# Kernel tuning notes

Hardware: AMD Instinct MI355X
Metric: run time of the kernel (lower is better)

Reference implementation:

```python
import jax, jax.numpy as jnp
import numpy as np
from jax import lax

T, B, D, H, C, G = 32, 512, 1024, 2048, 10, 16
BETA = 0.95
THRESH = 1.0


def _build_mask(key, out_f, in_f, p_intra=1.0, p_inter=0.15):
    ig, og = in_f // G, out_f // G
    same = (jnp.arange(out_f) // og)[:, None] == (jnp.arange(in_f) // ig)[None, :]
    probs = jnp.where(same, p_intra, p_inter)
    return (jax.random.uniform(key, (out_f, in_f)) < probs).astype(jnp.float32)


def setup_inputs() -> dict:
    key = jax.random.key(0)
    ks = jax.random.split(key, 12)
    def w(k, out_f, in_f):
        return jax.random.normal(k, (out_f, in_f), jnp.float32) * (1.0 / np.sqrt(in_f))
    return {
        'x_seq': jax.random.normal(ks[0], (T, B, D), jnp.float32),
        'w1': w(ks[1], H, D), 'b1': jax.random.normal(ks[2], (H,), jnp.float32) * 0.01,
        'mask1': _build_mask(ks[3], H, D),
        'w2': w(ks[4], H, H), 'b2': jax.random.normal(ks[5], (H,), jnp.float32) * 0.01,
        'mask2': _build_mask(ks[6], H, H),
        'w3': w(ks[7], H, H), 'b3': jax.random.normal(ks[8], (H,), jnp.float32) * 0.01,
        'mask3': _build_mask(ks[9], H, H),
        'w_out': w(ks[10], C, H), 'b_out': jax.random.normal(ks[11], (C,), jnp.float32) * 0.01,
    }


@jax.custom_vjp
def spike(x):
    # heaviside fire, fast_sigmoid(slope=25) surrogate gradient
    return (x > 0).astype(x.dtype)

def _spike_fwd(x):
    return spike(x), x

def _spike_bwd(x, g):
    return (g / (25.0 * jnp.abs(x) + 1.0) ** 2,)

spike.defvjp(_spike_fwd, _spike_bwd)


def _lif(cur, mem):
    # snntorch Leaky (reset-by-subtraction): reset from previous mem (detached)
    reset = lax.stop_gradient((mem > THRESH).astype(cur.dtype))
    mem = BETA * mem + cur - reset * THRESH
    spk = spike(mem - THRESH)
    return spk, mem


def reference(x_seq, w1, b1, mask1, w2, b2, mask2, w3, b3, mask3, w_out, b_out):
    # cache masked weights once (same math as per-step weight*mask)
    ew1, ew2, ew3 = w1 * mask1, w2 * mask2, w3 * mask3
    Bsz = x_seq.shape[1]
    mem1 = jnp.zeros((Bsz, H), x_seq.dtype)
    mem2 = jnp.zeros((Bsz, H), x_seq.dtype)
    mem3 = jnp.zeros((Bsz, H), x_seq.dtype)
    mem_o = jnp.zeros((Bsz, C), x_seq.dtype)
    ssum = jnp.zeros((Bsz, C), x_seq.dtype)

    def step(carry, x_t):
        mem1, mem2, mem3, mem_o, ssum = carry
        spk1, mem1 = _lif(x_t @ ew1.T + b1, mem1)
        spk2, mem2 = _lif(spk1 @ ew2.T + b2, mem2)
        spk3, mem3 = _lif(spk2 @ ew3.T + b3, mem3)
        spk_o, mem_o = _lif(spk3 @ w_out.T + b_out, mem_o)
        return (mem1, mem2, mem3, mem_o, ssum + spk_o), None

    (mem1, mem2, mem3, mem_o, ssum), _ = lax.scan(step, (mem1, mem2, mem3, mem_o, ssum), x_seq)
    return ssum
```

## Files before the change

kernel.cpp:

```cpp
#include <hip/hip_runtime.h>

#define TSTEPS 32
#define BSZ    512
#define DIN    1024
#define HID    2048
#define NCLS   10
#define BETA   0.95f
#define VTH    1.0f
#define SPKB   ((size_t)BSZ * (HID / 8))

typedef __attribute__((ext_vector_type(4))) float          f4;
typedef __attribute__((ext_vector_type(4))) float          f32x4;
typedef __attribute__((ext_vector_type(8))) __bf16         bf16x8;
typedef __attribute__((ext_vector_type(8))) unsigned short us8;
typedef __attribute__((ext_vector_type(4))) unsigned short us4;
typedef __attribute__((ext_vector_type(2))) unsigned int   u32x2;

__device__ inline unsigned short f2bf(float f) {
    unsigned u = __float_as_uint(f);
    u += 0x7FFF + ((u >> 16) & 1);
    return (unsigned short)(u >> 16);
}
__device__ inline float bf2f(unsigned short h) {
    return __uint_as_float(((unsigned)h) << 16);
}

__device__ __forceinline__ void split_f4pair(f4 v0, f4 v1, us8& o0, us8& o1, us8& o2) {
#pragma unroll
    for (int jj = 0; jj < 4; jj++) {
        float v = v0[jj];
        unsigned short h1 = f2bf(v); float r = v - bf2f(h1);
        unsigned short h2 = f2bf(r); float r2 = r - bf2f(h2);
        o0[jj] = h1; o1[jj] = h2; o2[jj] = f2bf(r2);
        v = v1[jj];
        h1 = f2bf(v); r = v - bf2f(h1);
        h2 = f2bf(r); r2 = r - bf2f(h2);
        o0[jj + 4] = h1; o1[jj + 4] = h2; o2[jj + 4] = f2bf(r2);
    }
}

__global__ __launch_bounds__(256)
void split3(const float* __restrict__ w, const float* __restrict__ m,
            unsigned short* __restrict__ h1, unsigned short* __restrict__ h2,
            unsigned short* __restrict__ h3, int n4)
{
    int i      = blockIdx.x * blockDim.x + threadIdx.x;
    int stride = gridDim.x * blockDim.x;
    for (; i < n4; i += stride) {
        f4 wv = ((const f4*)w)[i];
        f4 mv = ((const f4*)m)[i];
        us4 a, b, c;
#pragma unroll
        for (int j = 0; j < 4; j++) {
            float e  = wv[j] * mv[j];
            unsigned short x1 = f2bf(e);
            float r  = e - bf2f(x1);
            unsigned short x2 = f2bf(r);
            float r2 = r - bf2f(x2);
            a[j] = x1; b[j] = x2; c[j] = f2bf(r2);
        }
        ((us4*)h1)[i] = a;
        ((us4*)h2)[i] = b;
        ((us4*)h3)[i] = c;
    }
}

__global__ __launch_bounds__(256)
void split3q(const float* __restrict__ w, const float* __restrict__ m,
             unsigned short* __restrict__ q)
{
    const int NK = HID * HID;
    int gid = blockIdx.x * 256 + threadIdx.x;
    const int lane = gid & 63;
    const int t    = gid >> 6;
    const int kt   = t & (HID / 32 - 1);
    const int nt   = t >> 6;
    const int n = nt * 16 + (lane & 15);
    const int k = kt * 32 + (lane >> 4) * 8;
    const size_t src = (size_t)n * HID + k;
    f4 w0 = *(const f4*)(w + src),     w1v = *(const f4*)(w + src + 4);
    f4 m0 = *(const f4*)(m + src),     m1v = *(const f4*)(m + src + 4);
    us8 q0, q1, q2;
    split_f4pair(w0 * m0, w1v * m1v, q0, q1, q2);
    ((us8*)q)[gid]            = q0;
    ((us8*)(q + NK))[gid]     = q1;
    ((us8*)(q + 2 * NK))[gid] = q2;
}

__global__ __launch_bounds__(256)
void zerof(float* __restrict__ p, int n4)
{
    int i      = blockIdx.x * blockDim.x + threadIdx.x;
    int stride = gridDim.x * blockDim.x;
    f4 z = {0.f, 0.f, 0.f, 0.f};
    for (; i < n4; i += stride) ((f4*)p)[i] = z;
}

__device__ __forceinline__ void xsplit_dev(const float* __restrict__ xt,
                                           unsigned short* __restrict__ dst,
                                           int bid, int nblk, int tid)
{
    const int n4 = BSZ * DIN / 4;
    const int PS = BSZ * DIN;
    int i      = bid * 256 + tid;
    int stride = nblk * 256;
    for (; i < n4; i += stride) {
        f4 v = ((const f4*)xt)[i];
        us4 a, b, c;
#pragma unroll
        for (int j = 0; j < 4; j++) {
            float e = v[j];
            unsigned short x1 = f2bf(e);
            float r  = e - bf2f(x1);
            unsigned short x2 = f2bf(r);
            float r2 = r - bf2f(x2);
            a[j] = x1; b[j] = x2; c[j] = f2bf(r2);
        }
        ((us4*)(dst))[i]          = a;
        ((us4*)(dst + PS))[i]     = b;
        ((us4*)(dst + 2 * PS))[i] = c;
    }
}

__global__ __launch_bounds__(256)
void xsplit_k(const float* __restrict__ xt, unsigned short* __restrict__ dst)
{
    xsplit_dev(xt, dst, blockIdx.x, gridDim.x, threadIdx.x);
}

__device__ __forceinline__ void lif_epi(const f32x4 acc[2][2], const float* __restrict__ bias,
                                        float* __restrict__ memOut, unsigned char* __restrict__ sbits,
                                        int bm, int bn, int wm, int wn, int lane)
{
    const int fr = lane & 15;
#pragma unroll
    for (int fm = 0; fm < 2; fm++)
#pragma unroll
        for (int fn = 0; fn < 2; fn++) {
            const int n  = bn * 64 + wn * 32 + fn * 16 + fr;
            const float bv = bias[n];
            const int rbase = bm * 64 + wm * 32 + fm * 16 + (lane >> 4) * 4;
#pragma unroll
            for (int r = 0; r < 4; r++) {
                const int row = rbase + r;
                float* mp = memOut + (size_t)row * HID + n;
                float mo  = *mp;
                float m2  = BETA * mo + (acc[fm][fn][r] + bv) - ((mo > VTH) ? VTH : 0.f);
                *mp = m2;
                unsigned long long bal = __ballot(m2 > VTH);
                if (fr == 0) {
                    unsigned short bits = (unsigned short)(bal >> ((lane >> 4) * 16));
                    *(unsigned short*)(sbits + (size_t)row * (HID / 8) + bn * 8 + wn * 4 + fn * 2) = bits;
                }
            }
        }
}

__device__ __forceinline__ void lif_epi4b(const f32x4 (&acc)[4], const float* __restrict__ bias,
                                          float* __restrict__ memOut,
                                          unsigned char* __restrict__ sbitsOut,
                                          int bm, int bn, int wv, int lane)
{
    const int fr = lane & 15;
    const int n  = bn * 64 + wv * 16 + fr;
    const float bv = bias[n];
#pragma unroll
    for (int fm = 0; fm < 4; fm++) {
        const int rbase = bm * 64 + fm * 16 + (lane >> 4) * 4;
#pragma unroll
        for (int r = 0; r < 4; r++) {
            const int row = rbase + r;
            float* mp = memOut + (size_t)row * HID + n;
            float mo  = *mp;
            float m2  = BETA * mo + (acc[fm][r] + bv) - ((mo > VTH) ? VTH : 0.f);
            *mp = m2;
            unsigned long long bal = __ballot(m2 > VTH);
            if (fr == 0) {
                unsigned short bits = (unsigned short)(bal >> ((lane >> 4) * 16));
                *(unsigned short*)(sbitsOut + (size_t)row * (HID / 8) + bn * 8 + wv * 2) = bits;
            }
        }
    }
}

__device__ __forceinline__ void role_out_b(const unsigned char* __restrict__ sbits,
    const float* __restrict__ wo, const float* __restrict__ bo,
    float* __restrict__ memo, float* __restrict__ ssum, int b, int lane)
{
    const unsigned int bits = *(const unsigned int*)(sbits + (size_t)b * (HID / 8) + lane * 4);
    float acc[NCLS];
#pragma unroll
    for (int c = 0; c < NCLS; c++) {
        const f4* wrow = (const f4*)(wo + (size_t)c * HID + lane * 32);
        float s = 0.f;
#pragma unroll
        for (int q = 0; q < 8; q++) {
            f4 w = wrow[q];
#pragma unroll
            for (int i = 0; i < 4; i++)
                if ((bits >> (q * 4 + i)) & 1u) s += w[i];
        }
        acc[c] = s;
    }
#pragma unroll
    for (int c = 0; c < NCLS; c++)
#pragma unroll
        for (int m = 1; m < 64; m <<= 1) acc[c] += __shfl_xor(acc[c], m, 64);

    if (lane == 0) {
#pragma unroll
        for (int c = 0; c < NCLS; c++) {
            float mo  = memo[b * NCLS + c];
            float rst = (mo > VTH) ? VTH : 0.f;
            float m2  = BETA * mo + acc[c] + bo[c] - rst;
            memo[b * NCLS + c] = m2;
            if (m2 > VTH) ssum[b * NCLS + c] += 1.f;
        }
    }
}

__device__ __forceinline__ void role_l23b(unsigned char* smem,
    const unsigned char* __restrict__ sbitsIn,
    const unsigned short* __restrict__ Bp,
    const float* __restrict__ bias, float* __restrict__ memOut,
    unsigned char* __restrict__ sbitsOut, int rb, int tid)
{
    auto Bs = reinterpret_cast<unsigned short(*)[3][64 * 40]>(smem);
    const size_t PS = (size_t)HID * HID;

    const int bn = rb & 31, bm = rb >> 5;
    const int srow = tid >> 2, skq = tid & 3;
    const int lane = tid & 63, wv = tid >> 6;
    const int wm = wv >> 1, wn = wv & 1;
    const int fr = lane & 15, fk = (lane >> 4) * 8;
    const size_t bRow = (size_t)(bn * 64 + srow) * HID;
    const int sdst = srow * 40 + skq * 8;

    const unsigned char* aP0 = sbitsIn + (size_t)(bm * 64 + wm * 32 + fr) * (HID / 8);
    const unsigned char* aP1 = aP0 + (size_t)16 * (HID / 8);

    f32x4 acc[2][2] = {};
    us8 bb0, bb1, bb2;
    unsigned aw0, aw1;

    auto ldB = [&](int k0) {
        bb0 = *(const us8*)(Bp + bRow + k0 + skq * 8);
        bb1 = *(const us8*)(Bp + PS + bRow + k0 + skq * 8);
        bb2 = *(const us8*)(Bp + 2 * PS + bRow + k0 + skq * 8);
    };
    auto stage = [&](int nb) {
        *(us8*)&Bs[nb][0][sdst] = bb0;
        *(us8*)&Bs[nb][1][sdst] = bb1;
        *(us8*)&Bs[nb][2][sdst] = bb2;
    };

    ldB(0); stage(0);
    aw0 = *(const unsigned*)(aP0);
    aw1 = *(const unsigned*)(aP1);
    __syncthreads();

    const int nsteps = HID / 32;
    for (int s = 0; s < nsteps; s++) {
        const int buf = s & 1;
        const bool more = (s + 1 < nsteps);
        unsigned awn0 = 0, awn1 = 0;
        if (more) {
            ldB((s + 1) * 32);
            awn0 = *(const unsigned*)(aP0 + (s + 1) * 4);
            awn1 = *(const unsigned*)(aP1 + (s + 1) * 4);
        }

        bf16x8 af[2];
        {
            unsigned byt0 = aw0 >> fk, byt1 = aw1 >> fk;
            us8 e0, e1;
#pragma unroll
            for (int jj = 0; jj < 8; jj++) {
                e0[jj] = ((byt0 >> jj) & 1u) ? (unsigned short)0x3F80 : (unsigned short)0;
                e1[jj] = ((byt1 >> jj) & 1u) ? (unsigned short)0x3F80 : (unsigned short)0;
            }
            af[0] = *(bf16x8*)&e0;
            af[1] = *(bf16x8*)&e1;
        }

        bf16x8 bf[3][2];
#pragma unroll
        for (int fn = 0; fn < 2; fn++) {
            bf[0][fn] = *(const bf16x8*)&Bs[buf][0][(wn * 32 + fn * 16 + fr) * 40 + fk];
            bf[1][fn] = *(const bf16x8*)&Bs[buf][1][(wn * 32 + fn * 16 + fr) * 40 + fk];
            bf[2][fn] = *(const bf16x8*)&Bs[buf][2][(wn * 32 + fn * 16 + fr) * 40 + fk];
        }
#pragma unroll
        for (int fm = 0; fm < 2; fm++)
#pragma unroll
            for (int fn = 0; fn < 2; fn++) {
                acc[fm][fn] = __builtin_amdgcn_mfma_f32_16x16x32_bf16(af[fm], bf[0][fn], acc[fm][fn], 0, 0, 0);
                acc[fm][fn] = __builtin_amdgcn_mfma_f32_16x16x32_bf16(af[fm], bf[1][fn], acc[fm][fn], 0, 0, 0);
                acc[fm][fn] = __builtin_amdgcn_mfma_f32_16x16x32_bf16(af[fm], bf[2][fn], acc[fm][fn], 0, 0, 0);
            }

        if (more) { stage(buf ^ 1); aw0 = awn0; aw1 = awn1; }
        __syncthreads();
    }

    lif_epi(acc, bias, memOut, sbitsOut, bm, bn, wm, wn, lane);
}

__device__ __forceinline__ void role_l1p(unsigned char* smem,
    const unsigned short* __restrict__ Ap,
    const unsigned short* __restrict__ Wp,
    const float* __restrict__ bias, float* __restrict__ memOut,
    unsigned char* __restrict__ sbitsOut, int rb, int tid)
{
    auto As = reinterpret_cast<unsigned short(*)[64 * 40]>(smem);
    auto Bs = reinterpret_cast<unsigned short(*)[3][64 * 40]>(smem + 15360);
    const size_t APS = (size_t)BSZ * DIN;
    const size_t BPS = (size_t)HID * DIN;

    const int bn = rb & 31, bm = rb >> 5;
    const int srow = tid >> 2, skq = tid & 3;
    const int lane = tid & 63, wv = tid >> 6;
    const int wm = wv >> 1, wn = wv & 1;
    const int fr = lane & 15, fk = (lane >> 4) * 8;
    const size_t aRow = (size_t)(bm * 64 + srow) * DIN;
    const size_t bRow = (size_t)(bn * 64 + srow) * DIN;
    const int sdst = srow * 40 + skq * 8;

    f32x4 acc[2][2] = {};
    us8 aa0, aa1, aa2, bb0, bb1, bb2;

    auto ldnext = [&](int k0) {
        aa0 = *(const us8*)(Ap + aRow + k0 + skq * 8);
        aa1 = *(const us8*)(Ap + APS + aRow + k0 + skq * 8);
        aa2 = *(const us8*)(Ap + 2 * APS + aRow + k0 + skq * 8);
        bb0 = *(const us8*)(Wp + bRow + k0 + skq * 8);
        bb1 = *(const us8*)(Wp + BPS + bRow + k0 + skq * 8);
        bb2 = *(const us8*)(Wp + 2 * BPS + bRow + k0 + skq * 8);
    };
    auto stageA = [&]() {
        *(us8*)&As[0][sdst] = aa0;
        *(us8*)&As[1][sdst] = aa1;
        *(us8*)&As[2][sdst] = aa2;
    };
    auto stageB = [&](int nb) {
        *(us8*)&Bs[nb][0][sdst] = bb0;
        *(us8*)&Bs[nb][1][sdst] = bb1;
        *(us8*)&Bs[nb][2][sdst] = bb2;
    };

    ldnext(0); stageA(); stageB(0);
    __syncthreads();

    const int nsteps = DIN / 32;
    for (int s = 0; s < nsteps; s++) {
        const bool more = (s + 1 < nsteps);
        if (more) ldnext((s + 1) * 32);

        bf16x8 af[3][2], bf[3][2];
#pragma unroll
        for (int p = 0; p < 3; p++)
#pragma unroll
            for (int f = 0; f < 2; f++) {
                af[p][f] = *(const bf16x8*)&As[p][(wm * 32 + f * 16 + fr) * 40 + fk];
                bf[p][f] = *(const bf16x8*)&Bs[s & 1][p][(wn * 32 + f * 16 + fr) * 40 + fk];
            }
#pragma unroll
        for (int pa = 0; pa < 3; pa++)
#pragma unroll
            for (int pb = 0; pb < 3; pb++) {
                if (pa + pb <= 2) {
#pragma unroll
                    for (int fm = 0; fm < 2; fm++)
#pragma unroll
                        for (int fn = 0; fn < 2; fn++)
                            acc[fm][fn] = __builtin_amdgcn_mfma_f32_16x16x32_bf16(
                                af[pa][fm], bf[pb][fn], acc[fm][fn], 0, 0, 0);
                }
            }

        __syncthreads();
        if (more) { stageA(); stageB((s + 1) & 1); }
        __syncthreads();
    }

    lif_epi(acc, bias, memOut, sbitsOut, bm, bn, wm, wn, lane);
}

__global__ __launch_bounds__(256)
void snn_step2(const float* __restrict__ x,
               unsigned short* __restrict__ xp,
               const unsigned short* __restrict__ w1p, const float* __restrict__ b1,
               const unsigned short* __restrict__ w2p, const float* __restrict__ b2,
               const unsigned short* __restrict__ w3p, const float* __restrict__ b3,
               const float* __restrict__ wo, const float* __restrict__ bo,
               float* __restrict__ mem1, float* __restrict__ mem2, float* __restrict__ mem3,
               float* __restrict__ memo,
               unsigned char* __restrict__ spk1, unsigned char* __restrict__ spk2,
               unsigned char* __restrict__ spk3,
               float* __restrict__ ssum, int j)
{
    __shared__ __align__(16) unsigned char smem[46080];
    const int bid = blockIdx.x, tid = threadIdx.x;
    const size_t XSLOT = (size_t)3 * BSZ * DIN;

    if (bid < 256) {
        const int t = j;
        if (t <= TSTEPS - 1)
            role_l1p(smem, xp + (size_t)(t & 1) * XSLOT, w1p, b1, mem1,
                     spk1 + (size_t)(t & 1) * SPKB, bid, tid);
    } else if (bid < 512) {
        const int t = j - 1;
        if (t >= 0 && t <= TSTEPS - 1)
            role_l23b(smem, spk1 + (size_t)(t & 1) * SPKB, w2p, b2, mem2,
                      spk2 + (size_t)(t & 1) * SPKB, bid - 256, tid);
    } else if (bid < 768) {
        const int t = j - 2;
        if (t >= 0 && t <= TSTEPS - 1)
            role_l23b(smem, spk2 + (size_t)(t & 1) * SPKB, w3p, b3, mem3,
                      spk3 + (size_t)(t & 1) * SPKB, bid - 512, tid);
    } else {
        const int t1 = j + 1;
        if (t1 <= TSTEPS - 1)
            xsplit_dev(x + (size_t)t1 * BSZ * DIN,
                       xp + (size_t)(t1 & 1) * XSLOT, bid - 768, 128, tid);
        const int t = j - 3;
        if (t >= 0 && t <= TSTEPS - 1) {
            const int lane = tid & 63, wvi = tid >> 6;
            role_out_b(spk3 + (size_t)(t & 1) * SPKB, wo, bo, memo, ssum,
                       (bid - 768) * 4 + wvi, lane);
        }
    }
}


__device__ __forceinline__ void role_l23e(unsigned char* smem,
    const unsigned char* __restrict__ sbitsIn,
    const unsigned short* __restrict__ Bq,
    const float* __restrict__ bias, float* __restrict__ memOut,
    unsigned char* __restrict__ sbitsOut, int rb, int tid)
{
    u32x2* lut = (u32x2*)smem;
    if (tid < 16) {
        u32x2 e;
        e.x = ((tid & 1) ? 0x3F80u : 0u) | ((tid & 2) ? 0x3F800000u : 0u);
        e.y = ((tid & 4) ? 0x3F80u : 0u) | ((tid & 8) ? 0x3F800000u : 0u);
        lut[tid] = e;
    }
    __syncthreads();

    const int bn = rb & 31, bm = rb >> 5;
    const int lane = tid & 63, wv = tid >> 6;
    const int fr = lane & 15, fk = (lane >> 4) * 8;

    const size_t PSQ = (size_t)HID * HID / 8;
    const us8* bP0 = (const us8*)Bq + (size_t)(bn * 4 + wv) * (HID / 32) * 64 + lane;
    const us8* bP1 = bP0 + PSQ;
    const us8* bP2 = bP1 + PSQ;

    const unsigned char* aR = sbitsIn + (size_t)(bm * 64 + fr) * (HID / 8);

    f32x4 acc[4] = {};
    us8 bb[2][3];
    us4 awq[2][4];

#define LDB4(SET, S) do { const int sc_ = (S) < 64 ? (S) : 63;                 \
        bb[SET][0] = bP0[sc_ * 64];                                            \
        bb[SET][1] = bP1[sc_ * 64];                                            \
        bb[SET][2] = bP2[sc_ * 64]; } while (0)

#define LDA4(SET, G) do { const int gc_ = (G) < 16 ? (G) : 15;                 \
        awq[SET][0] = *(const us4*)(aR + 0 * 16 * (HID / 8) + gc_ * 16);       \
        awq[SET][1] = *(const us4*)(aR + 1 * 16 * (HID / 8) + gc_ * 16);       \
        awq[SET][2] = *(const us4*)(aR + 2 * 16 * (HID / 8) + gc_ * 16);       \
        awq[SET][3] = *(const us4*)(aR + 3 * 16 * (HID / 8) + gc_ * 16); } while (0)

#define EXPAND(AF, W) do { unsigned by_ = ((W) >> fk) & 0xFFu;                 \
        u32x2 lo_ = lut[by_ & 15u];                                            \
        u32x2 hi_ = lut[by_ >> 4];                                             \
        ((u32x2*)&(AF))[0] = lo_;                                              \
        ((u32x2*)&(AF))[1] = hi_; } while (0)

#define STEP(BSET, ASET, COMP) do {                                            \
        us8 a0_, a1_, a2_, a3_;                                                \
        EXPAND(a0_, awq[ASET][0][COMP]);                                       \
        EXPAND(a1_, awq[ASET][1][COMP]);                                       \
        EXPAND(a2_, awq[ASET][2][COMP]);                                       \
        EXPAND(a3_, awq[ASET][3][COMP]);                                       \
        bf16x8 b0_ = *(const bf16x8*)&bb[BSET][0];                             \
        bf16x8 b1_ = *(const bf16x8*)&bb[BSET][1];                             \
        bf16x8 b2_ = *(const bf16x8*)&bb[BSET][2];                             \
        bf16x8 fa0_ = *(const bf16x8*)&a0_;                                    \
        bf16x8 fa1_ = *(const bf16x8*)&a1_;                                    \
        bf16x8 fa2_ = *(const bf16x8*)&a2_;                                    \
        bf16x8 fa3_ = *(const bf16x8*)&a3_;                                    \
        acc[0] = __builtin_amdgcn_mfma_f32_16x16x32_bf16(fa0_, b0_, acc[0], 0, 0, 0); \
        acc[0] = __builtin_amdgcn_mfma_f32_16x16x32_bf16(fa0_, b1_, acc[0], 0, 0, 0); \
        acc[0] = __builtin_amdgcn_mfma_f32_16x16x32_bf16(fa0_, b2_, acc[0], 0, 0, 0); \
        acc[1] = __builtin_amdgcn_mfma_f32_16x16x32_bf16(fa1_, b0_, acc[1], 0, 0, 0); \
        acc[1] = __builtin_amdgcn_mfma_f32_16x16x32_bf16(fa1_, b1_, acc[1], 0, 0, 0); \
        acc[1] = __builtin_amdgcn_mfma_f32_16x16x32_bf16(fa1_, b2_, acc[1], 0, 0, 0); \
        acc[2] = __builtin_amdgcn_mfma_f32_16x16x32_bf16(fa2_, b0_, acc[2], 0, 0, 0); \
        acc[2] = __builtin_amdgcn_mfma_f32_16x16x32_bf16(fa2_, b1_, acc[2], 0, 0, 0); \
        acc[2] = __builtin_amdgcn_mfma_f32_16x16x32_bf16(fa2_, b2_, acc[2], 0, 0, 0); \
        acc[3] = __builtin_amdgcn_mfma_f32_16x16x32_bf16(fa3_, b0_, acc[3], 0, 0, 0); \
        acc[3] = __builtin_amdgcn_mfma_f32_16x16x32_bf16(fa3_, b1_, acc[3], 0, 0, 0); \
        acc[3] = __builtin_amdgcn_mfma_f32_16x16x32_bf16(fa3_, b2_, acc[3], 0, 0, 0); \
    } while (0)

    LDB4(0, 0); LDB4(1, 1);
    LDA4(0, 0); LDA4(1, 1);

    for (int g = 0; g < 16; g += 2) {
        const int s0 = g * 4;
        STEP(0, 0, 0); LDB4(0, s0 + 2);
        STEP(1, 0, 1); LDB4(1, s0 + 3);
        STEP(0, 0, 2); LDB4(0, s0 + 4);
        STEP(1, 0, 3); LDB4(1, s0 + 5);
        LDA4(0, g + 2);
        STEP(0, 1, 0); LDB4(0, s0 + 6);
        STEP(1, 1, 1); LDB4(1, s0 + 7);
        STEP(0, 1, 2); LDB4(0, s0 + 8);
        STEP(1, 1, 3); LDB4(1, s0 + 9);
        LDA4(1, g + 3);
    }

#undef LDB4
#undef LDA4
#undef EXPAND
#undef STEP

    lif_epi4b(acc, bias, memOut, sbitsOut, bm, bn, wv, lane);
}

__device__ __forceinline__ void role_l1s(unsigned char* smem,
    const unsigned short* __restrict__ Ap,
    const unsigned short* __restrict__ Wp,
    const float* __restrict__ bias, float* __restrict__ memOut,
    unsigned char* __restrict__ sbitsOut, int rb, int tid)
{
    auto As = reinterpret_cast<unsigned short(*)[64 * 40]>(smem);
    auto Bs = reinterpret_cast<unsigned short(*)[64 * 40]>(smem + 15360);
    const size_t APS = (size_t)BSZ * DIN;
    const size_t BPS = (size_t)HID * DIN;

    const int bn = rb & 31, bm = rb >> 5;
    const int srow = tid >> 2, skq = tid & 3;
    const int lane = tid & 63, wv = tid >> 6;
    const int wm = wv >> 1, wn = wv & 1;
    const int fr = lane & 15, fk = (lane >> 4) * 8;
    const size_t aRow = (size_t)(bm * 64 + srow) * DIN;
    const size_t bRow = (size_t)(bn * 64 + srow) * DIN;
    const int sdst = srow * 40 + skq * 8;

    f32x4 acc[2][2] = {};
    us8 aa0, aa1, aa2, bb0, bb1, bb2;

    auto ldnext = [&](int k0) {
        aa0 = *(const us8*)(Ap + aRow + k0 + skq * 8);
        aa1 = *(const us8*)(Ap + APS + aRow + k0 + skq * 8);
        aa2 = *(const us8*)(Ap + 2 * APS + aRow + k0 + skq * 8);
        bb0 = *(const us8*)(Wp + bRow + k0 + skq * 8);
        bb1 = *(const us8*)(Wp + BPS + bRow + k0 + skq * 8);
        bb2 = *(const us8*)(Wp + 2 * BPS + bRow + k0 + skq * 8);
    };
    auto stageAB = [&]() {
        *(us8*)&As[0][sdst] = aa0;
        *(us8*)&As[1][sdst] = aa1;
        *(us8*)&As[2][sdst] = aa2;
        *(us8*)&Bs[0][sdst] = bb0;
        *(us8*)&Bs[1][sdst] = bb1;
        *(us8*)&Bs[2][sdst] = bb2;
    };

    ldnext(0); stageAB();
    __syncthreads();

    const int nsteps = DIN / 32;
    for (int s = 0; s < nsteps; s++) {
        const bool more = (s + 1 < nsteps);
        if (more) ldnext((s + 1) * 32);

        bf16x8 af[3][2], bf[3][2];
#pragma unroll
        for (int p = 0; p < 3; p++)
#pragma unroll
            for (int f = 0; f < 2; f++) {
                af[p][f] = *(const bf16x8*)&As[p][(wm * 32 + f * 16 + fr) * 40 + fk];
                bf[p][f] = *(const bf16x8*)&Bs[p][(wn * 32 + f * 16 + fr) * 40 + fk];
            }
#pragma unroll
        for (int pa = 0; pa < 3; pa++)
#pragma unroll
            for (int pb = 0; pb < 3; pb++) {
                if (pa + pb <= 2) {
#pragma unroll
                    for (int fm = 0; fm < 2; fm++)
#pragma unroll
                        for (int fn = 0; fn < 2; fn++)
                            acc[fm][fn] = __builtin_amdgcn_mfma_f32_16x16x32_bf16(
                                af[pa][fm], bf[pb][fn], acc[fm][fn], 0, 0, 0);
                }
            }

        __syncthreads();
        if (more) stageAB();
        __syncthreads();
    }

    lif_epi(acc, bias, memOut, sbitsOut, bm, bn, wm, wn, lane);
}

__global__ __launch_bounds__(256, 4)
void snn_step4(const float* __restrict__ x,
               unsigned short* __restrict__ xp,
               const unsigned short* __restrict__ w1p, const float* __restrict__ b1,
               const unsigned short* __restrict__ w2q, const float* __restrict__ b2,
               const unsigned short* __restrict__ w3q, const float* __restrict__ b3,
               const float* __restrict__ wo, const float* __restrict__ bo,
               float* __restrict__ mem1, float* __restrict__ mem2, float* __restrict__ mem3,
               float* __restrict__ memo,
               unsigned char* __restrict__ spk1, unsigned char* __restrict__ spk2,
               unsigned char* __restrict__ spk3,
               float* __restrict__ ssum, int j)
{
    __shared__ __align__(16) unsigned char smem[30720];
    const int bid = blockIdx.x, tid = threadIdx.x;
    const size_t XSLOT = (size_t)3 * BSZ * DIN;

    if (bid < 256) {
        const int t = j;
        if (t <= TSTEPS - 1)
            role_l1s(smem, xp + (size_t)(t & 1) * XSLOT, w1p, b1, mem1,
                     spk1 + (size_t)(t & 1) * SPKB, bid, tid);
    } else if (bid < 512) {
        const int t = j - 1;
        if (t >= 0 && t <= TSTEPS - 1)
            role_l23e(smem, spk1 + (size_t)(t & 1) * SPKB, w2q, b2, mem2,
                      spk2 + (size_t)(t & 1) * SPKB, bid - 256, tid);
    } else if (bid < 768) {
        const int t = j - 2;
        if (t >= 0 && t <= TSTEPS - 1)
            role_l23e(smem, spk2 + (size_t)(t & 1) * SPKB, w3q, b3, mem3,
                      spk3 + (size_t)(t & 1) * SPKB, bid - 512, tid);
    } else {
        const int t1 = j + 1;
        if (t1 <= TSTEPS - 1)
            xsplit_dev(x + (size_t)t1 * BSZ * DIN,
                       xp + (size_t)(t1 & 1) * XSLOT, bid - 768, 256, tid);
        const int t = j - 3;
        if (t >= 0 && t <= TSTEPS - 1) {
            const int lane = tid & 63, wvi = tid >> 6;
            if (wvi < 2)
                role_out_b(spk3 + (size_t)(t & 1) * SPKB, wo, bo, memo, ssum,
                           (bid - 768) * 2 + wvi, lane);
        }
    }
}

extern "C" void kernel_launch(void* const* d_in, const int* in_sizes, int n_in,
                              void* d_out, int out_size, void* d_ws, size_t ws_size,
                              hipStream_t stream)
{
    const float* x  = (const float*)d_in[0];
    const float* w1 = (const float*)d_in[1];
    const float* b1 = (const float*)d_in[2];
    const float* m1 = (const float*)d_in[3];
    const float* w2 = (const float*)d_in[4];
    const float* b2 = (const float*)d_in[5];
    const float* m2 = (const float*)d_in[6];
    const float* w3 = (const float*)d_in[7];
    const float* b3 = (const float*)d_in[8];
    const float* m3 = (const float*)d_in[9];
    const float* wo = (const float*)d_in[10];
    const float* bo = (const float*)d_in[11];
    float* out = (float*)d_out;

    const size_t planeB  = (size_t)HID * HID * 2;
    const size_t plane1B = (size_t)HID * DIN * 2;
    const size_t planeXB = (size_t)BSZ * DIN * 2;
    const size_t memB    = (size_t)BSZ * HID * 4;
    const size_t memoB   = (size_t)BSZ * NCLS * 4;
    const size_t spk2B   = 2 * SPKB;

    unsigned char* base = (unsigned char*)d_ws;

    const size_t needV4 = 6 * planeB + 3 * plane1B + 6 * planeXB
                        + 3 * memB + memoB + 3 * spk2B + 4096;

    const int nW1  = HID * DIN / 4;
    const size_t HH = (size_t)HID * HID;
    const size_t HD = (size_t)HID * DIN;

    if (ws_size >= needV4) {
        unsigned short* w2q = (unsigned short*)base;
        unsigned short* w3q = (unsigned short*)(base + 3 * planeB);
        unsigned short* w1p = (unsigned short*)(base + 6 * planeB);
        unsigned short* xp  = (unsigned short*)(base + 6 * planeB + 3 * plane1B);
        unsigned char* mbase = base + 6 * planeB + 3 * plane1B + 6 * planeXB;
        float* mem1 = (float*)(mbase);
        float* mem2 = (float*)(mbase + memB);
        float* mem3 = (float*)(mbase + 2 * memB);
        float* memo = (float*)(mbase + 3 * memB);
        unsigned char* spk1 = mbase + 3 * memB + memoB;
        unsigned char* spk2 = spk1 + spk2B;
        unsigned char* spk3 = spk2 + spk2B;

        split3q<<<2048, 256, 0, stream>>>(w2, m2, w2q);
        split3q<<<2048, 256, 0, stream>>>(w3, m3, w3q);
        split3<<<1024, 256, 0, stream>>>(w1, m1, w1p, w1p + HD, w1p + 2 * HD, nW1);
        xsplit_k<<<256, 256, 0, stream>>>(x, xp);

        zerof<<<1024, 256, 0, stream>>>(mem1, (int)((3 * memB + memoB) / 16));
        zerof<<<8, 256, 0, stream>>>(out, (BSZ * NCLS) / 4);

        for (int j = 0; j <= TSTEPS + 2; j++) {
            snn_step4<<<1024, 256, 0, stream>>>(x, xp, w1p, b1, w2q, b2, w3q, b3,
                                                wo, bo, mem1, mem2, mem3, memo,
                                                spk1, spk2, spk3, out, j);
        }
        return;
    }

    const size_t needV2 = 6 * planeB + 3 * plane1B + 6 * planeXB
                        + 3 * memB + memoB + 3 * spk2B;
    if (ws_size < needV2) return;

    unsigned short* w2p = (unsigned short*)base;
    unsigned short* w3p = (unsigned short*)(base + 3 * planeB);
    unsigned short* w1p = (unsigned short*)(base + 6 * planeB);
    unsigned short* xp  = (unsigned short*)(base + 6 * planeB + 3 * plane1B);
    unsigned char* mbase = base + 6 * planeB + 3 * plane1B + 6 * planeXB;
    float* mem1 = (float*)(mbase);
    float* mem2 = (float*)(mbase + memB);
    float* mem3 = (float*)(mbase + 2 * memB);
    float* memo = (float*)(mbase + 3 * memB);
    unsigned char* spk1 = mbase + 3 * memB + memoB;
    unsigned char* spk2 = spk1 + spk2B;
    unsigned char* spk3 = spk2 + spk2B;

    const int nW23 = HID * HID / 4;
    split3<<<1024, 256, 0, stream>>>(w2, m2, w2p, w2p + HH, w2p + 2 * HH, nW23);
    split3<<<1024, 256, 0, stream>>>(w3, m3, w3p, w3p + HH, w3p + 2 * HH, nW23);
    split3<<<1024, 256, 0, stream>>>(w1, m1, w1p, w1p + HD, w1p + 2 * HD, nW1);
    xsplit_k<<<256, 256, 0, stream>>>(x, xp);

    zerof<<<1024, 256, 0, stream>>>(mem1, (int)((3 * memB + memoB) / 16));
    zerof<<<8, 256, 0, stream>>>(out, (BSZ * NCLS) / 4);

    for (int j = 0; j <= TSTEPS + 2; j++) {
        snn_step2<<<896, 256, 0, stream>>>(x, xp, w1p, b1, w2p, b2, w3p, b3,
                                           wo, bo, mem1, mem2, mem3, memo,
                                           spk1, spk2, spk3, out, j);
    }
}
```

Measured before the change: 1.738 ms.

## Halve layer-2/3 tile height, prefragment x for direct MFMA loads, raise occupancy

Layers 2 and 3 now use 32-row tiles, so their block count doubles to 512 per layer and the grid grows to 1536 blocks, with launch bounds raised to 6 blocks per CU. The spike-bit inner loop is restructured to load 32-bit words per 32-wide K step and expand them through the LUT. The x split now writes a layout matching the MFMA fragments, so layer 1 reads A directly from global memory instead of staging it in LDS, which halves shared memory. This targets more parallelism and less LDS traffic, at the cost of lower reuse of the B operand per block and more global A reads.

Result: slower. 3.177 ms (+82.8%).

```diff
diff --git a/kernel.cpp b/kernel.cpp
--- a/kernel.cpp
+++ b/kernel.cpp
@@ -128,6 +128,35 @@
     xsplit_dev(xt, dst, blockIdx.x, gridDim.x, threadIdx.x);
 }
 
+__device__ __forceinline__ void xsplitq_dev(const float* __restrict__ xt,
+                                            unsigned short* __restrict__ dstu,
+                                            int bid, int tid)
+{
+    us8* dst = (us8*)dstu;
+    const int gid  = bid * 256 + tid;
+    const int lane = gid & 63;
+    const int t2   = gid >> 6;
+    const int kt   = t2 & 31;
+    const int rt   = t2 >> 5;
+    const int n = rt * 16 + (lane & 15);
+    const int k = kt * 32 + (lane >> 4) * 8;
+    const size_t src = (size_t)n * DIN + k;
+    f4 v0 = *(const f4*)(xt + src);
+    f4 v1 = *(const f4*)(xt + src + 4);
+    us8 q0, q1, q2;
+    split_f4pair(v0, v1, q0, q1, q2);
+    const size_t XPS = (size_t)BSZ * DIN / 8;
+    dst[gid]            = q0;
+    dst[XPS + gid]      = q1;
+    dst[2 * XPS + gid]  = q2;
+}
+
+__global__ __launch_bounds__(256)
+void xsplitq_k(const float* __restrict__ xt, unsigned short* __restrict__ dst)
+{
+    xsplitq_dev(xt, dst, blockIdx.x, threadIdx.x);
+}
+
 __device__ __forceinline__ void lif_epi(const f32x4 acc[2][2], const float* __restrict__ bias,
                                         float* __restrict__ memOut, unsigned char* __restrict__ sbits,
                                         int bm, int bn, int wm, int wn, int lane)
@@ -156,7 +185,7 @@
         }
 }
 
-__device__ __forceinline__ void lif_epi4b(const f32x4 (&acc)[4], const float* __restrict__ bias,
+__device__ __forceinline__ void lif_epi2b(const f32x4 (&acc)[2], const float* __restrict__ bias,
                                           float* __restrict__ memOut,
                                           unsigned char* __restrict__ sbitsOut,
                                           int bm, int bn, int wv, int lane)
@@ -165,8 +194,8 @@
     const int n  = bn * 64 + wv * 16 + fr;
     const float bv = bias[n];
 #pragma unroll
-    for (int fm = 0; fm < 4; fm++) {
-        const int rbase = bm * 64 + fm * 16 + (lane >> 4) * 4;
+    for (int fm = 0; fm < 2; fm++) {
+        const int rbase = bm * 32 + fm * 16 + (lane >> 4) * 4;
 #pragma unroll
         for (int r = 0; r < 4; r++) {
             const int row = rbase + r;
@@ -433,7 +462,7 @@
 }
 
 
-__device__ __forceinline__ void role_l23e(unsigned char* smem,
+__device__ __forceinline__ void role_l23g(unsigned char* smem,
     const unsigned char* __restrict__ sbitsIn,
     const unsigned short* __restrict__ Bq,
     const float* __restrict__ bias, float* __restrict__ memOut,
@@ -457,137 +486,123 @@
     const us8* bP1 = bP0 + PSQ;
     const us8* bP2 = bP1 + PSQ;
 
-    const unsigned char* aR = sbitsIn + (size_t)(bm * 64 + fr) * (HID / 8);
-
-    f32x4 acc[4] = {};
-    us8 bb[2][3];
-    us4 awq[2][4];
-
-#define LDB4(SET, S) do { const int sc_ = (S) < 64 ? (S) : 63;                 \
-        bb[SET][0] = bP0[sc_ * 64];                                            \
-        bb[SET][1] = bP1[sc_ * 64];                                            \
-        bb[SET][2] = bP2[sc_ * 64]; } while (0)
-
-#define LDA4(SET, G) do { const int gc_ = (G) < 16 ? (G) : 15;                 \
-        awq[SET][0] = *(const us4*)(aR + 0 * 16 * (HID / 8) + gc_ * 16);       \
-        awq[SET][1] = *(const us4*)(aR + 1 * 16 * (HID / 8) + gc_ * 16);       \
-        awq[SET][2] = *(const us4*)(aR + 2 * 16 * (HID / 8) + gc_ * 16);       \
-        awq[SET][3] = *(const us4*)(aR + 3 * 16 * (HID / 8) + gc_ * 16); } while (0)
-
-#define EXPAND(AF, W) do { unsigned by_ = ((W) >> fk) & 0xFFu;                 \
+    const unsigned char* aP0 = sbitsIn + (size_t)(bm * 32 + fr) * (HID / 8);
+    const unsigned char* aP1 = aP0 + (size_t)16 * (HID / 8);
+
+    f32x4 acc[2] = {};
+    us8 bbA0, bbA1, bbA2, bbB0, bbB1, bbB2;
+    unsigned awA0, awA1, awB0, awB1;
+    us8 afA0, afA1, afB0, afB1;
+
+#define LDBA_(S) do { const int sc_ = (S) < 64 ? (S) : 63;                     \
+        bbA0 = bP0[sc_ * 64]; bbA1 = bP1[sc_ * 64]; bbA2 = bP2[sc_ * 64]; } while (0)
+#define LDBB_(S) do { const int sc_ = (S) < 64 ? (S) : 63;                     \
+        bbB0 = bP0[sc_ * 64]; bbB1 = bP1[sc_ * 64]; bbB2 = bP2[sc_ * 64]; } while (0)
+#define LDAWA_(S) do { const int sc_ = (S) < 64 ? (S) : 63;                    \
+        awA0 = *(const unsigned*)(aP0 + sc_ * 4);                              \
+        awA1 = *(const unsigned*)(aP1 + sc_ * 4); } while (0)
+#define LDAWB_(S) do { const int sc_ = (S) < 64 ? (S) : 63;                    \
+        awB0 = *(const unsigned*)(aP0 + sc_ * 4);                              \
+        awB1 = *(const unsigned*)(aP1 + sc_ * 4); } while (0)
+#define EXPW_(AF, W) do { unsigned by_ = ((W) >> fk) & 0xFFu;                  \
         u32x2 lo_ = lut[by_ & 15u];                                            \
         u32x2 hi_ = lut[by_ >> 4];                                             \
         ((u32x2*)&(AF))[0] = lo_;                                              \
         ((u32x2*)&(AF))[1] = hi_; } while (0)
-
-#define STEP(BSET, ASET, COMP) do {                                            \
-        us8 a0_, a1_, a2_, a3_;                                                \
-        EXPAND(a0_, awq[ASET][0][COMP]);                                       \
-        EXPAND(a1_, awq[ASET][1][COMP]);                                       \
-        EXPAND(a2_, awq[ASET][2][COMP]);                                       \
-        EXPAND(a3_, awq[ASET][3][COMP]);                                       \
-        bf16x8 b0_ = *(const bf16x8*)&bb[BSET][0];                             \
-        bf16x8 b1_ = *(const bf16x8*)&bb[BSET][1];                             \
-        bf16x8 b2_ = *(const bf16x8*)&bb[BSET][2];                             \
-        bf16x8 fa0_ = *(const bf16x8*)&a0_;                                    \
-        bf16x8 fa1_ = *(const bf16x8*)&a1_;                                    \
-        bf16x8 fa2_ = *(const bf16x8*)&a2_;                                    \
-        bf16x8 fa3_ = *(const bf16x8*)&a3_;                                    \
-        acc[0] = __builtin_amdgcn_mfma_f32_16x16x32_bf16(fa0_, b0_, acc[0], 0, 0, 0); \
-        acc[0] = __builtin_amdgcn_mfma_f32_16x16x32_bf16(fa0_, b1_, acc[0], 0, 0, 0); \
-        acc[0] = __builtin_amdgcn_mfma_f32_16x16x32_bf16(fa0_, b2_, acc[0], 0, 0, 0); \
-        acc[1] = __builtin_amdgcn_mfma_f32_16x16x32_bf16(fa1_, b0_, acc[1], 0, 0, 0); \
-        acc[1] = __builtin_amdgcn_mfma_f32_16x16x32_bf16(fa1_, b1_, acc[1], 0, 0, 0); \
-        acc[1] = __builtin_amdgcn_mfma_f32_16x16x32_bf16(fa1_, b2_, acc[1], 0, 0, 0); \
-        acc[2] = __builtin_amdgcn_mfma_f32_16x16x32_bf16(fa2_, b0_, acc[2], 0, 0, 0); \
-        acc[2] = __builtin_amdgcn_mfma_f32_16x16x32_bf16(fa2_, b1_, acc[2], 0, 0, 0); \
-        acc[2] = __builtin_amdgcn_mfma_f32_16x16x32_bf16(fa2_, b2_, acc[2], 0, 0, 0); \
-        acc[3] = __builtin_amdgcn_mfma_f32_16x16x32_bf16(fa3_, b0_, acc[3], 0, 0, 0); \
-        acc[3] = __builtin_amdgcn_mfma_f32_16x16x32_bf16(fa3_, b1_, acc[3], 0, 0, 0); \
-        acc[3] = __builtin_amdgcn_mfma_f32_16x16x32_bf16(fa3_, b2_, acc[3], 0, 0, 0); \
-    } while (0)
-
-    LDB4(0, 0); LDB4(1, 1);
-    LDA4(0, 0); LDA4(1, 1);
-
-    for (int g = 0; g < 16; g += 2) {
-        const int s0 = g * 4;
-        STEP(0, 0, 0); LDB4(0, s0 + 2);
-        STEP(1, 0, 1); LDB4(1, s0 + 3);
-        STEP(0, 0, 2); LDB4(0, s0 + 4);
-        STEP(1, 0, 3); LDB4(1, s0 + 5);
-        LDA4(0, g + 2);
-        STEP(0, 1, 0); LDB4(0, s0 + 6);
-        STEP(1, 1, 1); LDB4(1, s0 + 7);
-        STEP(0, 1, 2); LDB4(0, s0 + 8);
-        STEP(1, 1, 3); LDB4(1, s0 + 9);
-        LDA4(1, g + 3);
-    }
-
-#undef LDB4
-#undef LDA4
-#undef EXPAND
-#undef STEP
-
-    lif_epi4b(acc, bias, memOut, sbitsOut, bm, bn, wv, lane);
-}
-
-__device__ __forceinline__ void role_l1s(unsigned char* smem,
-    const unsigned short* __restrict__ Ap,
+#define MM6_(A0, A1, B0, B1, B2) do {                                          \
+        bf16x8 b0_ = *(const bf16x8*)&(B0);                                    \
+        bf16x8 b1_ = *(const bf16x8*)&(B1);                                    \
+        bf16x8 b2_ = *(const bf16x8*)&(B2);                                    \
+        bf16x8 a0_ = *(const bf16x8*)&(A0);                                    \
+        bf16x8 a1_ = *(const bf16x8*)&(A1);                                    \
+        acc[0] = __builtin_amdgcn_mfma_f32_16x16x32_bf16(a0_, b0_, acc[0], 0, 0, 0); \
+        acc[1] = __builtin_amdgcn_mfma_f32_16x16x32_bf16(a1_, b0_, acc[1], 0, 0, 0); \
+        acc[0] = __builtin_amdgcn_mfma_f32_16x16x32_bf16(a0_, b1_, acc[0], 0, 0, 0); \
+        acc[1] = __builtin_amdgcn_mfma_f32_16x16x32_bf16(a1_, b1_, acc[1], 0, 0, 0); \
+        acc[0] = __builtin_amdgcn_mfma_f32_16x16x32_bf16(a0_, b2_, acc[0], 0, 0, 0); \
+        acc[1] = __builtin_amdgcn_mfma_f32_16x16x32_bf16(a1_, b2_, acc[1], 0, 0, 0); } while (0)
+
+    LDBA_(0); LDBB_(1);
+    LDAWA_(0); LDAWB_(1);
+    EXPW_(afA0, awA0); EXPW_(afA1, awA1);
+
+    for (int s = 0; s < 64; s += 2) {
+        LDAWA_(s + 2);
+        EXPW_(afB0, awB0); EXPW_(afB1, awB1);
+        MM6_(afA0, afA1, bbA0, bbA1, bbA2);
+        LDBA_(s + 2);
+        LDAWB_(s + 3);
+        EXPW_(afA0, awA0); EXPW_(afA1, awA1);
+        MM6_(afB0, afB1, bbB0, bbB1, bbB2);
+        LDBB_(s + 3);
+    }
+
+#undef LDBA_
+#undef LDBB_
+#undef LDAWA_
+#undef LDAWB_
+#undef EXPW_
+#undef MM6_
+
+    lif_epi2b(acc, bias, memOut, sbitsOut, bm, bn, wv, lane);
+}
+
+__device__ __forceinline__ void role_l1f(unsigned char* smem,
+    const unsigned short* __restrict__ xq,
     const unsigned short* __restrict__ Wp,
     const float* __restrict__ bias, float* __restrict__ memOut,
     unsigned char* __restrict__ sbitsOut, int rb, int tid)
 {
-    auto As = reinterpret_cast<unsigned short(*)[64 * 40]>(smem);
-    auto Bs = reinterpret_cast<unsigned short(*)[64 * 40]>(smem + 15360);
-    const size_t APS = (size_t)BSZ * DIN;
+    auto Bs = reinterpret_cast<unsigned short(*)[64 * 40]>(smem);
     const size_t BPS = (size_t)HID * DIN;
+    const size_t XPS = (size_t)BSZ * DIN / 8;
+    const us8* xq8 = (const us8*)xq;
 
     const int bn = rb & 31, bm = rb >> 5;
     const int srow = tid >> 2, skq = tid & 3;
-    const int lane = tid & 63, wv = tid >> 6;
-    const int wm = wv >> 1, wn = wv & 1;
+    const int lane = tid & 63, wvv = tid >> 6;
+    const int wm = wvv >> 1, wn = wvv & 1;
     const int fr = lane & 15, fk = (lane >> 4) * 8;
-    const size_t aRow = (size_t)(bm * 64 + srow) * DIN;
     const size_t bRow = (size_t)(bn * 64 + srow) * DIN;
     const int sdst = srow * 40 + skq * 8;
+    const int rt0 = bm * 4 + wm * 2;
 
     f32x4 acc[2][2] = {};
-    us8 aa0, aa1, aa2, bb0, bb1, bb2;
-
-    auto ldnext = [&](int k0) {
-        aa0 = *(const us8*)(Ap + aRow + k0 + skq * 8);
-        aa1 = *(const us8*)(Ap + APS + aRow + k0 + skq * 8);
-        aa2 = *(const us8*)(Ap + 2 * APS + aRow + k0 + skq * 8);
+    us8 bb0, bb1, bb2;
+
+    auto ldB = [&](int k0) {
         bb0 = *(const us8*)(Wp + bRow + k0 + skq * 8);
         bb1 = *(const us8*)(Wp + BPS + bRow + k0 + skq * 8);
         bb2 = *(const us8*)(Wp + 2 * BPS + bRow + k0 + skq * 8);
     };
-    auto stageAB = [&]() {
-        *(us8*)&As[0][sdst] = aa0;
-        *(us8*)&As[1][sdst] = aa1;
-        *(us8*)&As[2][sdst] = aa2;
+    auto stageB = [&]() {
         *(us8*)&Bs[0][sdst] = bb0;
         *(us8*)&Bs[1][sdst] = bb1;
         *(us8*)&Bs[2][sdst] = bb2;
     };
 
-    ldnext(0); stageAB();
+    ldB(0); stageB();
     __syncthreads();
 
     const int nsteps = DIN / 32;
     for (int s = 0; s < nsteps; s++) {
         const bool more = (s + 1 < nsteps);
-        if (more) ldnext((s + 1) * 32);
-
-        bf16x8 af[3][2], bf[3][2];
+        if (more) ldB((s + 1) * 32);
+
+        us8 axr[3][2];
 #pragma unroll
         for (int p = 0; p < 3; p++)
 #pragma unroll
-            for (int f = 0; f < 2; f++) {
-                af[p][f] = *(const bf16x8*)&As[p][(wm * 32 + f * 16 + fr) * 40 + fk];
+            for (int f = 0; f < 2; f++)
+                axr[p][f] = xq8[(size_t)p * XPS + (size_t)((rt0 + f) * 32 + s) * 64 + lane];
+
+        bf16x8 bf[3][2];
+#pragma unroll
+        for (int p = 0; p < 3; p++)
+#pragma unroll
+            for (int f = 0; f < 2; f++)
                 bf[p][f] = *(const bf16x8*)&Bs[p][(wn * 32 + f * 16 + fr) * 40 + fk];
-            }
+
 #pragma unroll
         for (int pa = 0; pa < 3; pa++)
 #pragma unroll
@@ -598,21 +613,21 @@
 #pragma unroll
                         for (int fn = 0; fn < 2; fn++)
                             acc[fm][fn] = __builtin_amdgcn_mfma_f32_16x16x32_bf16(
-                                af[pa][fm], bf[pb][fn], acc[fm][fn], 0, 0, 0);
+                                *(const bf16x8*)&axr[pa][fm], bf[pb][fn], acc[fm][fn], 0, 0, 0);
                 }
             }
 
         __syncthreads();
-        if (more) stageAB();
+        if (more) stageB();
         __syncthreads();
     }
 
     lif_epi(acc, bias, memOut, sbitsOut, bm, bn, wm, wn, lane);
 }
 
-__global__ __launch_bounds__(256, 4)
-void snn_step4(const float* __restrict__ x,
-               unsigned short* __restrict__ xp,
+__global__ __launch_bounds__(256, 6)
+void snn_step6(const float* __restrict__ x,
+               unsigned short* __restrict__ xq,
                const unsigned short* __restrict__ w1p, const float* __restrict__ b1,
                const unsigned short* __restrict__ w2q, const float* __restrict__ b2,
                const unsigned short* __restrict__ w3q, const float* __restrict__ b3,
@@ -623,36 +638,36 @@
                unsigned char* __restrict__ spk3,
                float* __restrict__ ssum, int j)
 {
-    __shared__ __align__(16) unsigned char smem[30720];
+    __shared__ __align__(16) unsigned char smem[15360];
     const int bid = blockIdx.x, tid = threadIdx.x;
     const size_t XSLOT = (size_t)3 * BSZ * DIN;
 
     if (bid < 256) {
         const int t = j;
         if (t <= TSTEPS - 1)
-            role_l1s(smem, xp + (size_t)(t & 1) * XSLOT, w1p, b1, mem1,
+            role_l1f(smem, xq + (size_t)(t & 1) * XSLOT, w1p, b1, mem1,
                      spk1 + (size_t)(t & 1) * SPKB, bid, tid);
-    } else if (bid < 512) {
+    } else if (bid < 768) {
         const int t = j - 1;
         if (t >= 0 && t <= TSTEPS - 1)
-            role_l23e(smem, spk1 + (size_t)(t & 1) * SPKB, w2q, b2, mem2,
+            role_l23g(smem, spk1 + (size_t)(t & 1) * SPKB, w2q, b2, mem2,
                       spk2 + (size_t)(t & 1) * SPKB, bid - 256, tid);
-    } else if (bid < 768) {
+    } else if (bid < 1280) {
         const int t = j - 2;
         if (t >= 0 && t <= TSTEPS - 1)
-            role_l23e(smem, spk2 + (size_t)(t & 1) * SPKB, w3q, b3, mem3,
-                      spk3 + (size_t)(t & 1) * SPKB, bid - 512, tid);
+            role_l23g(smem, spk2 + (size_t)(t & 1) * SPKB, w3q, b3, mem3,
+                      spk3 + (size_t)(t & 1) * SPKB, bid - 768, tid);
     } else {
         const int t1 = j + 1;
         if (t1 <= TSTEPS - 1)
-            xsplit_dev(x + (size_t)t1 * BSZ * DIN,
-                       xp + (size_t)(t1 & 1) * XSLOT, bid - 768, 256, tid);
+            xsplitq_dev(x + (size_t)t1 * BSZ * DIN,
+                        xq + (size_t)(t1 & 1) * XSLOT, bid - 1280, tid);
         const int t = j - 3;
         if (t >= 0 && t <= TSTEPS - 1) {
             const int lane = tid & 63, wvi = tid >> 6;
             if (wvi < 2)
                 role_out_b(spk3 + (size_t)(t & 1) * SPKB, wo, bo, memo, ssum,
-                           (bid - 768) * 2 + wvi, lane);
+                           (bid - 1280) * 2 + wvi, lane);
         }
     }
 }
@@ -684,18 +699,18 @@
 
     unsigned char* base = (unsigned char*)d_ws;
 
-    const size_t needV4 = 6 * planeB + 3 * plane1B + 6 * planeXB
+    const size_t needV6 = 6 * planeB + 3 * plane1B + 6 * planeXB
                         + 3 * memB + memoB + 3 * spk2B + 4096;
 
     const int nW1  = HID * DIN / 4;
     const size_t HH = (size_t)HID * HID;
     const size_t HD = (size_t)HID * DIN;
 
-    if (ws_size >= needV4) {
+    if (ws_size >= needV6) {
         unsigned short* w2q = (unsigned short*)base;
         unsigned short* w3q = (unsigned short*)(base + 3 * planeB);
         unsigned short* w1p = (unsigned short*)(base + 6 * planeB);
-        unsigned short* xp  = (unsigned short*)(base + 6 * planeB + 3 * plane1B);
+        unsigned short* xq  = (unsigned short*)(base + 6 * planeB + 3 * plane1B);
         unsigned char* mbase = base + 6 * planeB + 3 * plane1B + 6 * planeXB;
         float* mem1 = (float*)(mbase);
         float* mem2 = (float*)(mbase + memB);
@@ -708,13 +723,13 @@
         split3q<<<2048, 256, 0, stream>>>(w2, m2, w2q);
         split3q<<<2048, 256, 0, stream>>>(w3, m3, w3q);
         split3<<<1024, 256, 0, stream>>>(w1, m1, w1p, w1p + HD, w1p + 2 * HD, nW1);
-        xsplit_k<<<256, 256, 0, stream>>>(x, xp);
+        xsplitq_k<<<256, 256, 0, stream>>>(x, xq);
 
         zerof<<<1024, 256, 0, stream>>>(mem1, (int)((3 * memB + memoB) / 16));
         zerof<<<8, 256, 0, stream>>>(out, (BSZ * NCLS) / 4);
 
         for (int j = 0; j <= TSTEPS + 2; j++) {
-            snn_step4<<<1024, 256, 0, stream>>>(x, xp, w1p, b1, w2q, b2, w3q, b3,
+            snn_step6<<<1536, 256, 0, stream>>>(x, xq, w1p, b1, w2q, b2, w3q, b3,
                                                 wo, bo, mem1, mem2, mem3, memo,
                                                 spk1, spk2, spk3, out, j);
         }
```
